# Optimization experiments

Measured on AMD Instinct MI355X. Metric: run time of the kernel, lower is better.

Reference implementation:

```python
import jax, jax.numpy as jnp
import numpy as np

# mamba-130m backbone dims. NOTE: the original torch code wires Conv1d(1,8,...) into a
# 768-d Mamba (a latent bug); we resolve it by making the downsample conv emit d_model.
B, L_IN = 2, 135000
D_MODEL, N_LAYERS = 768, 24
D_INNER, D_STATE, D_CONV, DT_RANK = 1536, 16, 4, 48
K_DS, S_DS = 32, 32
LATENT = 64


def setup_inputs() -> dict:
    key = jax.random.key(0)
    ks = jax.random.split(key, 16)
    s = 0.02
    dt = jax.random.uniform(ks[12], (N_LAYERS, D_INNER), minval=1e-3, maxval=1e-1)
    return {
        "x": jax.random.normal(ks[0], (B, 1, L_IN), dtype=jnp.float32),
        "conv_w": jax.random.normal(ks[1], (D_MODEL, 1, K_DS)) * s,
        "conv_b": jnp.zeros((D_MODEL,)),
        "norm_w": jnp.ones((N_LAYERS, D_MODEL)),
        "in_proj_w": jax.random.normal(ks[2], (N_LAYERS, 2 * D_INNER, D_MODEL)) * s,
        "conv1d_w": jax.random.normal(ks[3], (N_LAYERS, D_INNER, D_CONV)) * s,
        "conv1d_b": jnp.zeros((N_LAYERS, D_INNER)),
        "x_proj_w": jax.random.normal(ks[4], (N_LAYERS, DT_RANK + 2 * D_STATE, D_INNER)) * s,
        "dt_proj_w": jax.random.normal(ks[5], (N_LAYERS, D_INNER, DT_RANK)) * s,
        "dt_proj_b": dt + jnp.log(-jnp.expm1(-dt)),  # inverse-softplus init
        "A_log": jnp.log(jnp.broadcast_to(jnp.arange(1, D_STATE + 1, dtype=jnp.float32), (N_LAYERS, D_INNER, D_STATE)) + 0.0),
        "D_skip": jnp.ones((N_LAYERS, D_INNER)),
        "out_proj_w": jax.random.normal(ks[6], (N_LAYERS, D_MODEL, D_INNER)) * s,
        "norm_f_w": jnp.ones((D_MODEL,)),
        "proj_w": jax.random.normal(ks[7], (LATENT, D_MODEL)) * s,
        "proj_b": jnp.zeros((LATENT,)),
        "ln_w": jnp.ones((LATENT,)),
        "ln_b": jnp.zeros((LATENT,)),
    }


def _rmsnorm(x, w):
    return x * jax.lax.rsqrt(jnp.mean(x * x, axis=-1, keepdims=True) + 1e-5) * w


def _mamba_layer(h, p):
    norm_w, in_w, cw, cb, xp_w, dt_w, dt_b, A_log, Dp, out_w = p
    xz = jnp.einsum('btd,ed->bte', _rmsnorm(h, norm_w), in_w)  # e = 2*d_inner
    u, z = jnp.split(xz, 2, axis=-1)
    # causal depthwise conv over time
    uc = jax.lax.conv_general_dilated(jnp.transpose(u, (0, 2, 1)), cw[:, None, :], (1,),
                                      [(D_CONV - 1, 0)], dimension_numbers=('NCH', 'OIH', 'NCH'),
                                      feature_group_count=D_INNER)
    u = jax.nn.silu(jnp.transpose(uc + cb[None, :, None], (0, 2, 1)))  # (B,T,d_inner)
    proj = jnp.einsum('btd,ed->bte', u, xp_w)
    dt, Bm, Cm = jnp.split(proj, [DT_RANK, DT_RANK + D_STATE], axis=-1)
    delta = jax.nn.softplus(jnp.einsum('btr,dr->btd', dt, dt_w) + dt_b)
    A = -jnp.exp(A_log)  # (d_inner, d_state)

    def step(hc, inp):
        u_t, d_t, b_t, c_t = inp  # (B,d_inner),(B,d_inner),(B,d_state),(B,d_state)
        hc = jnp.exp(d_t[..., None] * A) * hc + (d_t * u_t)[..., None] * b_t[:, None, :]
        return hc, jnp.einsum('bds,bs->bd', hc, c_t)

    h0 = jnp.zeros((u.shape[0], D_INNER, D_STATE), dtype=u.dtype)
    tfirst = lambda a: jnp.transpose(a, (1, 0, 2))
    _, ys = jax.lax.scan(step, h0, (tfirst(u), tfirst(delta), tfirst(Bm), tfirst(Cm)))
    y = (jnp.transpose(ys, (1, 0, 2)) + u * Dp) * jax.nn.silu(z)
    return h + jnp.einsum('bte,de->btd', y, out_w), None


def _forward(x, conv_w, conv_b, norm_w, in_proj_w, conv1d_w, conv1d_b, x_proj_w, dt_proj_w,
             dt_proj_b, A_log, D_skip, out_proj_w, norm_f_w, proj_w, proj_b, ln_w, ln_b):
    # downsample: (B,1,135000) -> (B,768,4218) -> (B,4218,768)
    xds = jax.lax.conv_general_dilated(x, conv_w, (S_DS,), 'VALID',
                                       dimension_numbers=('NCH', 'OIH', 'NCH')) + conv_b[None, :, None]
    h = jnp.transpose(xds, (0, 2, 1))
    params = (norm_w, in_proj_w, conv1d_w, conv1d_b, x_proj_w, dt_proj_w, dt_proj_b, A_log, D_skip, out_proj_w)
    h, _ = jax.lax.scan(_mamba_layer, h, params)
    h = _rmsnorm(h, norm_f_w)  # last_hidden_state
    pooled = h.mean(axis=1)  # mean pooling
    zed = pooled @ proj_w.T + proj_b
    mu = zed.mean(-1, keepdims=True)
    var = ((zed - mu) ** 2).mean(-1, keepdims=True)
    return (zed - mu) * jax.lax.rsqrt(var + 1e-5) * ln_w + ln_b  # dropout is identity in eval


def reference(x, conv_w, conv_b, norm_w, in_proj_w, conv1d_w, conv1d_b, x_proj_w, dt_proj_w,
              dt_proj_b, A_log, D_skip, out_proj_w, norm_f_w, proj_w, proj_b, ln_w, ln_b):
    return _forward(x, conv_w, conv_b, norm_w, in_proj_w, conv1d_w, conv1d_b, x_proj_w,
                    dt_proj_w, dt_proj_b, A_log, D_skip, out_proj_w, norm_f_w, proj_w,
                    proj_b, ln_w, ln_b)
```

## Files before the change

### kernel.cpp

```cpp
#include <hip/hip_runtime.h>
#include <hip/hip_bf16.h>
#include <math.h>

#define TT 4218
#define BB 2
#define DM 768
#define DI 1536
#define DS 16
#define DTR 48
#define LC 64
#define NCHUNK 66
#define ROWS (BB*TT)
#define NLAYER 24

typedef short short8 __attribute__((ext_vector_type(8)));
typedef float f32x4 __attribute__((ext_vector_type(4)));

__device__ __forceinline__ float silu_f(float x) { return x / (1.0f + __expf(-x)); }
__device__ __forceinline__ float softplus_f(float x) {
  return (x > 15.0f) ? x : log1pf(__expf(x));
}
__device__ __forceinline__ unsigned short f2bf(float x) {
  unsigned int u = __float_as_uint(x);
  u = (u + 0x7fffu + ((u >> 16) & 1u)) >> 16;
  return (unsigned short)u;
}
__device__ __forceinline__ float bf2f(unsigned short s) {
  return __uint_as_float(((unsigned int)s) << 16);
}

__global__ __launch_bounds__(256)
void k_f2bf(const float4* __restrict__ in, ushort4* __restrict__ out, int n4) {
  int i = blockIdx.x*256 + threadIdx.x;
  if (i >= n4) return;
  float4 v = in[i];
  ushort4 o;
  o.x = f2bf(v.x); o.y = f2bf(v.y); o.z = f2bf(v.z); o.w = f2bf(v.w);
  out[i] = o;
}

__global__ __launch_bounds__(256)
void k_cvt_dtw(const float* __restrict__ in, unsigned short* __restrict__ out, int n) {
  int i = blockIdx.x*256 + threadIdx.x;
  if (i >= n) return;
  int col = i & 63, row = i >> 6;
  out[i] = (col < DTR) ? f2bf(in[row*DTR + col]) : (unsigned short)0;
}

__global__ __launch_bounds__(256)
void k_zero_dtpad(unsigned short* __restrict__ fdt) {
  int i = blockIdx.x*256 + threadIdx.x;
  if (i >= ROWS*16) return;
  int r = i >> 4, c = i & 15;
  fdt[(size_t)r*64 + DTR + c] = 0;
}

__global__ __launch_bounds__(256)
void k_conv_ds(const float* __restrict__ x, const float* __restrict__ cw,
               const float* __restrict__ cb, float* __restrict__ h) {
  int bt = blockIdx.x;
  int b = bt / TT, t = bt % TT;
  __shared__ float xs[32];
  int tid = threadIdx.x;
  if (tid < 32) xs[tid] = x[(size_t)b*135000 + (size_t)t*32 + tid];
  __syncthreads();
  for (int d = tid; d < DM; d += 256) {
    float s = cb[d];
    const float* w = cw + d*32;
    #pragma unroll
    for (int k = 0; k < 32; ++k) s = fmaf(xs[k], w[k], s);
    h[(size_t)bt*DM + d] = s;
  }
}

__global__ __launch_bounds__(256)
void k_rmsnorm(const float* __restrict__ in, const float* __restrict__ w,
               unsigned short* __restrict__ out) {
  int row = blockIdx.x, tid = threadIdx.x;
  const float* xp = in + (size_t)row*DM;
  float v0 = xp[tid], v1 = xp[tid+256], v2 = xp[tid+512];
  float ss = v0*v0 + v1*v1 + v2*v2;
  #pragma unroll
  for (int off = 32; off > 0; off >>= 1) ss += __shfl_down(ss, off, 64);
  __shared__ float sred[4];
  if ((tid & 63) == 0) sred[tid >> 6] = ss;
  __syncthreads();
  float tot = sred[0] + sred[1] + sred[2] + sred[3];
  float sc = rsqrtf(tot * (1.0f/DM) + 1e-5f);
  unsigned short* op = out + (size_t)row*DM;
  op[tid]     = f2bf(v0*sc*w[tid]);
  op[tid+256] = f2bf(v1*sc*w[tid+256]);
  op[tid+512] = f2bf(v2*sc*w[tid+512]);
}

#define GLL(g, l) __builtin_amdgcn_global_load_lds( \
    (const __attribute__((address_space(1))) void*)(g), \
    (__attribute__((address_space(3))) void*)(l), 16, 0, 0)

template<int MODE>
__global__ __launch_bounds__(256)
void k_gemm_bf(const unsigned short* __restrict__ A,
               const unsigned short* __restrict__ W,
               const float* __restrict__ bias,
               float* __restrict__ Cf,
               unsigned short* __restrict__ Cb0, unsigned short* __restrict__ Cb1,
               int ldc, int M, int N, int K) {
  const int m0 = blockIdx.x*128, n0 = blockIdx.y*128;
  if (m0 >= M) return;
  __shared__ unsigned short As[128*32];
  __shared__ unsigned short Ws[128*32];
  const int tid = threadIdx.x;
  const int lane = tid & 63;
  const int wave = tid >> 6;
  const int wm = (wave >> 1)*64, wn = (wave & 1)*64;

  const int sA = tid & 3;
  const int r0 = tid >> 2;
  const int r1 = r0 + 64;
  const int seg0 = sA ^ ((r0 >> 1) & 3);
  const int seg1 = sA ^ ((r1 >> 1) & 3);
  const unsigned short* gA0 = A + (size_t)min(m0+r0, M-1)*K + seg0*8;
  const unsigned short* gA1 = A + (size_t)min(m0+r1, M-1)*K + seg1*8;
  const unsigned short* gW0 = W + (size_t)min(n0+r0, N-1)*K + seg0*8;
  const unsigned short* gW1 = W + (size_t)min(n0+r1, N-1)*K + seg1*8;
  unsigned short* lA0 = As + tid*8;
  unsigned short* lA1 = As + (tid+256)*8;
  unsigned short* lW0 = Ws + tid*8;
  unsigned short* lW1 = Ws + (tid+256)*8;

  f32x4 acc[4][4];
  #pragma unroll
  for (int i = 0; i < 4; ++i)
    #pragma unroll
    for (int j = 0; j < 4; ++j) acc[i][j] = (f32x4){0.f,0.f,0.f,0.f};

  const int lr = lane & 15, kg = lane >> 4;
  const int sw = (kg ^ ((lr >> 1) & 3)) * 8;
  const int aoff = (wm + lr)*32 + sw;
  const int boff = (wn + lr)*32 + sw;

  for (int k0 = 0; k0 < K; k0 += 32) {
    GLL(gA0, lA0); GLL(gA1, lA1);
    GLL(gW0, lW0); GLL(gW1, lW1);
    gA0 += 32; gA1 += 32; gW0 += 32; gW1 += 32;
    __syncthreads();
    short8 af[4], bfr[4];
    #pragma unroll
    for (int i = 0; i < 4; ++i) {
      af[i]  = *(const short8*)(As + aoff + i*512);
      bfr[i] = *(const short8*)(Ws + boff + i*512);
    }
    #pragma unroll
    for (int i = 0; i < 4; ++i)
      #pragma unroll
      for (int j = 0; j < 4; ++j)
        acc[i][j] = __builtin_amdgcn_mfma_f32_16x16x32_bf16(af[i], bfr[j], acc[i][j], 0, 0, 0);
    __syncthreads();
  }

  #pragma unroll
  for (int i = 0; i < 4; ++i) {
    int gr0 = m0 + wm + i*16 + kg*4;
    #pragma unroll
    for (int j = 0; j < 4; ++j) {
      int gc = n0 + wn + j*16 + lr;
      if (gc >= N) continue;
      #pragma unroll
      for (int r = 0; r < 4; ++r) {
        int gr = gr0 + r;
        if (gr >= M) continue;
        float v = acc[i][j][r];
        if (MODE == 0) {
          if (gc < DI) Cb0[(size_t)gr*ldc + gc] = f2bf(v);
          else         Cb1[(size_t)gr*ldc + gc - DI] = f2bf(v);
        } else if (MODE == 1) {
          Cf[(size_t)gr*ldc + gc] += v;
        } else {
          Cf[(size_t)gr*ldc + gc] = softplus_f(v + bias[gc]);
        }
      }
    }
  }
}

__global__ __launch_bounds__(256)
void k_gemm_xp(const unsigned short* __restrict__ A,
               const unsigned short* __restrict__ W,
               float* __restrict__ Cpr, unsigned short* __restrict__ Cdt,
               int M) {
  __shared__ unsigned short As[64*64];
  __shared__ unsigned short Ws[80*64];
  const int tid = threadIdx.x;
  const int m0 = blockIdx.x*64;
  const int lane = tid & 63;
  const int wave = tid >> 6;
  const int K = DI;

  const int rA0 = tid >> 3,        gA0s = (tid & 7) ^ (rA0 & 7);
  const int rA1 = (tid+256) >> 3,  gA1s = ((tid+256) & 7) ^ (rA1 & 7);
  const unsigned short* gA0 = A + (size_t)min(m0+rA0, M-1)*K + gA0s*8;
  const unsigned short* gA1 = A + (size_t)min(m0+rA1, M-1)*K + gA1s*8;
  unsigned short* lA0 = As + tid*8;
  unsigned short* lA1 = As + (size_t)(tid+256)*8;
  const int rW0 = tid >> 3,        gW0s = (tid & 7) ^ (rW0 & 7);
  const int rW1 = (tid+256) >> 3,  gW1s = ((tid+256) & 7) ^ (rW1 & 7);
  const int rW2 = (tid+512) >> 3,  gW2s = ((tid+512) & 7) ^ (rW2 & 7);
  const unsigned short* gW0 = W + (size_t)rW0*K + gW0s*8;
  const unsigned short* gW1 = W + (size_t)rW1*K + gW1s*8;
  const unsigned short* gW2 = W + (size_t)min(rW2,79)*K + gW2s*8;
  unsigned short* lW0 = Ws + tid*8;
  unsigned short* lW1 = Ws + (size_t)(tid+256)*8;
  unsigned short* lW2 = Ws + (size_t)(tid+512)*8;
  const bool doW2 = (tid < 128);

  f32x4 acc[5];
  #pragma unroll
  for (int j = 0; j < 5; ++j) acc[j] = (f32x4){0.f,0.f,0.f,0.f};

  const int lr = lane & 15, kg = lane >> 4;
  const int rowA = wave*16 + lr;

  for (int k0 = 0; k0 < K; k0 += 64) {
    GLL(gA0, lA0); GLL(gA1, lA1);
    GLL(gW0, lW0); GLL(gW1, lW1);
    if (doW2) GLL(gW2, lW2);
    gA0 += 64; gA1 += 64; gW0 += 64; gW1 += 64; gW2 += 64;
    __syncthreads();
    #pragma unroll
    for (int ks = 0; ks < 2; ++ks) {
      const int G = ks*4 + kg;
      short8 af = *(const short8*)(As + ((size_t)rowA*8 + (G ^ (rowA & 7)))*8);
      #pragma unroll
      for (int j = 0; j < 5; ++j) {
        const int rw = j*16 + lr;
        short8 bf = *(const short8*)(Ws + ((size_t)rw*8 + (G ^ (rw & 7)))*8);
        acc[j] = __builtin_amdgcn_mfma_f32_16x16x32_bf16(af, bf, acc[j], 0, 0, 0);
      }
    }
    __syncthreads();
  }

  #pragma unroll
  for (int j = 0; j < 5; ++j) {
    int gc = j*16 + lr;
    #pragma unroll
    for (int r = 0; r < 4; ++r) {
      int gr = m0 + wave*16 + kg*4 + r;
      if (gr >= M) continue;
      float v = acc[j][r];
      Cpr[(size_t)gr*80 + gc] = v;
      if (gc < DTR) Cdt[(size_t)gr*64 + gc] = f2bf(v);
    }
  }
}

__global__ __launch_bounds__(256)
void k_dwconv(const unsigned short* __restrict__ U0, const float* __restrict__ cw,
              const float* __restrict__ cb, unsigned short* __restrict__ ubf) {
  size_t i4 = (size_t)blockIdx.x*256 + threadIdx.x;
  if (i4 >= (size_t)ROWS*DI/4) return;
  size_t base = i4*4;
  int d = (int)(base % DI);
  size_t bt = base / DI;
  int t = (int)(bt % TT);
  float4 cbv = *(const float4*)(cb + d);
  float s0 = cbv.x, s1 = cbv.y, s2 = cbv.z, s3 = cbv.w;
  float4 w0v = *(const float4*)(cw + (size_t)(d+0)*4);
  float4 w1v = *(const float4*)(cw + (size_t)(d+1)*4);
  float4 w2v = *(const float4*)(cw + (size_t)(d+2)*4);
  float4 w3v = *(const float4*)(cw + (size_t)(d+3)*4);
  const float* w0 = (const float*)&w0v;
  const float* w1 = (const float*)&w1v;
  const float* w2 = (const float*)&w2v;
  const float* w3 = (const float*)&w3v;
  #pragma unroll
  for (int k = 0; k < 4; ++k) {
    int tt = t - 3 + k;
    if (tt < 0) continue;
    ushort4 uu = *(const ushort4*)(U0 + (bt - 3 + k)*DI + d);
    s0 = fmaf(bf2f(uu.x), w0[k], s0);
    s1 = fmaf(bf2f(uu.y), w1[k], s1);
    s2 = fmaf(bf2f(uu.z), w2[k], s2);
    s3 = fmaf(bf2f(uu.w), w3[k], s3);
  }
  ushort4 o4;
  o4.x = f2bf(silu_f(s0)); o4.y = f2bf(silu_f(s1));
  o4.z = f2bf(silu_f(s2)); o4.w = f2bf(silu_f(s3));
  *(ushort4*)(ubf + base) = o4;
}

__global__ __launch_bounds__(256)
void k_scan1(const float* __restrict__ delta, const unsigned short* __restrict__ u,
             const float* __restrict__ proj, const float* __restrict__ A_log,
             float* __restrict__ P, float* __restrict__ H) {
  int c = blockIdx.x, b = blockIdx.z;
  int d = blockIdx.y * 256 + threadIdx.x;
  float A[DS];
  {
    const float4* a4 = (const float4*)(A_log + (size_t)d*DS);
    #pragma unroll
    for (int q = 0; q < 4; ++q) {
      float4 v = a4[q];
      A[q*4+0] = -__expf(v.x); A[q*4+1] = -__expf(v.y);
      A[q*4+2] = -__expf(v.z); A[q*4+3] = -__expf(v.w);
    }
  }
  float h[DS] = {};
  float sdl = 0.0f;
  int t0 = c * LC, t1 = min(t0 + LC, TT);
  for (int t = t0; t < t1; ++t) {
    size_t bt = (size_t)b*TT + t;
    float dl = delta[bt*DI + d];
    float du = dl * bf2f(u[bt*DI + d]);
    const float4* pb4 = (const float4*)(proj + bt*80 + DTR);
    float4 B0 = pb4[0], B1 = pb4[1], B2 = pb4[2], B3 = pb4[3];
    float Bv[DS] = {B0.x,B0.y,B0.z,B0.w, B1.x,B1.y,B1.z,B1.w,
                    B2.x,B2.y,B2.z,B2.w, B3.x,B3.y,B3.z,B3.w};
    sdl += dl;
    #pragma unroll
    for (int s = 0; s < DS; ++s) {
      float e = __expf(dl * A[s]);
      h[s] = fmaf(e, h[s], du * Bv[s]);
    }
  }
  size_t o = (((size_t)c*BB + b)*DI + d)*DS;
  #pragma unroll
  for (int q = 0; q < 4; ++q) {
    float4 pv, hv;
    pv.x = __expf(sdl*A[q*4+0]); pv.y = __expf(sdl*A[q*4+1]);
    pv.z = __expf(sdl*A[q*4+2]); pv.w = __expf(sdl*A[q*4+3]);
    hv.x = h[q*4+0]; hv.y = h[q*4+1]; hv.z = h[q*4+2]; hv.w = h[q*4+3];
    *(float4*)(P + o + q*4) = pv;
    *(float4*)(H + o + q*4) = hv;
  }
}

__global__ __launch_bounds__(256)
void k_scan2(float* __restrict__ P, float* __restrict__ H) {
  int i = blockIdx.x*256 + threadIdx.x;
  const size_t CH = (size_t)BB*DI*DS;
  size_t o = (size_t)i;
  float carry = 0.0f;
  float p0 = P[o],      h0 = H[o];
  float p1 = P[o + CH], h1 = H[o + CH];
  for (int c = 0; c < NCHUNK; ++c) {
    float p2 = 0.0f, h2 = 0.0f;
    if (c + 2 < NCHUNK) { size_t o2 = o + 2*CH; p2 = P[o2]; h2 = H[o2]; }
    H[o] = carry;
    carry = fmaf(p0, carry, h0);
    p0 = p1; h0 = h1; p1 = p2; h1 = h2;
    o += CH;
  }
}

__global__ __launch_bounds__(256)
void k_scan3(const float* __restrict__ delta, const unsigned short* __restrict__ u,
             const unsigned short* __restrict__ z, const float* __restrict__ proj,
             const float* __restrict__ A_log, const float* __restrict__ Dskip,
             const float* __restrict__ H, unsigned short* __restrict__ y) {
  int c = blockIdx.x, b = blockIdx.z;
  int d = blockIdx.y * 256 + threadIdx.x;
  float A[DS];
  {
    const float4* a4 = (const float4*)(A_log + (size_t)d*DS);
    #pragma unroll
    for (int q = 0; q < 4; ++q) {
      float4 v = a4[q];
      A[q*4+0] = -__expf(v.x); A[q*4+1] = -__expf(v.y);
      A[q*4+2] = -__expf(v.z); A[q*4+3] = -__expf(v.w);
    }
  }
  float h[DS];
  size_t o = (((size_t)c*BB + b)*DI + d)*DS;
  #pragma unroll
  for (int q = 0; q < 4; ++q) {
    float4 hv = *(const float4*)(H + o + q*4);
    h[q*4+0] = hv.x; h[q*4+1] = hv.y; h[q*4+2] = hv.z; h[q*4+3] = hv.w;
  }
  float Dd = Dskip[d];
  int t0 = c * LC, t1 = min(t0 + LC, TT);
  for (int t = t0; t < t1; ++t) {
    size_t bt = (size_t)b*TT + t;
    float dl = delta[bt*DI + d];
    float uu = bf2f(u[bt*DI + d]);
    float du = dl * uu;
    const float4* pb4 = (const float4*)(proj + bt*80 + DTR);
    float4 B0 = pb4[0], B1 = pb4[1], B2 = pb4[2], B3 = pb4[3];
    float4 C0 = pb4[4], C1 = pb4[5], C2 = pb4[6], C3 = pb4[7];
    float Bv[DS] = {B0.x,B0.y,B0.z,B0.w, B1.x,B1.y,B1.z,B1.w,
                    B2.x,B2.y,B2.z,B2.w, B3.x,B3.y,B3.z,B3.w};
    float Cv[DS] = {C0.x,C0.y,C0.z,C0.w, C1.x,C1.y,C1.z,C1.w,
                    C2.x,C2.y,C2.z,C2.w, C3.x,C3.y,C3.z,C3.w};
    float yt = 0.0f;
    #pragma unroll
    for (int s = 0; s < DS; ++s) {
      float e = __expf(dl * A[s]);
      h[s] = fmaf(e, h[s], du * Bv[s]);
      yt = fmaf(h[s], Cv[s], yt);
    }
    float zz = bf2f(z[bt*DI + d]);
    y[bt*DI + d] = f2bf((yt + uu*Dd) * silu_f(zz));
  }
}

__global__ __launch_bounds__(256)
void k_poolpart(const unsigned short* __restrict__ hn, float* __restrict__ pp) {
  int seg = blockIdx.x, b = blockIdx.z;
  int d = blockIdx.y*256 + threadIdx.x;
  int t0 = seg*132, t1 = min(t0 + 132, TT);
  float s = 0.0f;
  for (int t = t0; t < t1; ++t) s += bf2f(hn[((size_t)b*TT + t)*DM + d]);
  pp[((size_t)b*32 + seg)*DM + d] = s;
}

__global__ __launch_bounds__(256)
void k_head(const float* __restrict__ pp, const float* __restrict__ pw,
            const float* __restrict__ pb, const float* __restrict__ lnw,
            const float* __restrict__ lnb, float* __restrict__ out) {
  int b = blockIdx.x, tid = threadIdx.x;
  __shared__ float pooled[DM];
  for (int d = tid; d < DM; d += 256) {
    float s = 0.0f;
    for (int seg = 0; seg < 32; ++seg) s += pp[((size_t)b*32 + seg)*DM + d];
    pooled[d] = s * (1.0f/(float)TT);
  }
  __syncthreads();
  __shared__ float zed[64];
  if (tid < 64) {
    float s = pb[tid];
    const float* w = pw + (size_t)tid*DM;
    for (int d = 0; d < DM; ++d) s = fmaf(pooled[d], w[d], s);
    zed[tid] = s;
  }
  __syncthreads();
  __shared__ float mv[2];
  if (tid == 0) {
    float mu = 0.0f;
    for (int l = 0; l < 64; ++l) mu += zed[l];
    mu *= (1.0f/64.0f);
    float var = 0.0f;
    for (int l = 0; l < 64; ++l) { float dd = zed[l]-mu; var += dd*dd; }
    var *= (1.0f/64.0f);
    mv[0] = mu; mv[1] = rsqrtf(var + 1e-5f);
  }
  __syncthreads();
  if (tid < 64) out[b*64 + tid] = (zed[tid]-mv[0])*mv[1]*lnw[tid] + lnb[tid];
}

extern "C" void kernel_launch(void* const* d_in, const int* in_sizes, int n_in,
                              void* d_out, int out_size, void* d_ws, size_t ws_size,
                              hipStream_t stream) {
  (void)in_sizes; (void)n_in; (void)out_size; (void)ws_size;
  const float* x    = (const float*)d_in[0];
  const float* cw   = (const float*)d_in[1];
  const float* cb   = (const float*)d_in[2];
  const float* nw   = (const float*)d_in[3];
  const float* inw  = (const float*)d_in[4];
  const float* c1w  = (const float*)d_in[5];
  const float* c1b  = (const float*)d_in[6];
  const float* xpw  = (const float*)d_in[7];
  const float* dtw  = (const float*)d_in[8];
  const float* dtb  = (const float*)d_in[9];
  const float* alog = (const float*)d_in[10];
  const float* dsk  = (const float*)d_in[11];
  const float* outw = (const float*)d_in[12];
  const float* nfw  = (const float*)d_in[13];
  const float* pw   = (const float*)d_in[14];
  const float* pb   = (const float*)d_in[15];
  const float* lnw  = (const float*)d_in[16];
  const float* lnb  = (const float*)d_in[17];

  char* wsb = (char*)d_ws;
  size_t o = 0;
  float* f_h  = (float*)(wsb + o); o += (size_t)ROWS*DM*4;
  float* f_pr = (float*)(wsb + o); o += (size_t)ROWS*80*4;
  float* f_dl = (float*)(wsb + o); o += (size_t)ROWS*DI*4;
  float* f_P  = (float*)(wsb + o); o += (size_t)NCHUNK*BB*DI*DS*4;
  float* f_H  = (float*)(wsb + o); o += (size_t)NCHUNK*BB*DI*DS*4;
  float* f_pp = (float*)(wsb + o); o += (size_t)BB*32*DM*4;
  unsigned short* hn_bf = (unsigned short*)(wsb + o); o += (size_t)ROWS*DM*2;
  unsigned short* u0_bf = (unsigned short*)(wsb + o); o += (size_t)ROWS*DI*2;
  unsigned short* z_bf  = (unsigned short*)(wsb + o); o += (size_t)ROWS*DI*2;
  unsigned short* u_bf  = (unsigned short*)(wsb + o); o += (size_t)ROWS*DI*2;
  unsigned short* y_bf  = (unsigned short*)(wsb + o); o += (size_t)ROWS*DI*2;
  unsigned short* f_dt  = (unsigned short*)(wsb + o); o += (size_t)ROWS*64*2;
  unsigned short* w_in  = (unsigned short*)(wsb + o); o += (size_t)2*DI*DM*2;
  unsigned short* w_xp  = (unsigned short*)(wsb + o); o += (size_t)NLAYER*80*DI*2;
  unsigned short* w_out = (unsigned short*)(wsb + o); o += (size_t)NLAYER*DM*DI*2;
  unsigned short* w_dt  = (unsigned short*)(wsb + o); o += (size_t)NLAYER*DI*64*2;

  k_conv_ds<<<ROWS, 256, 0, stream>>>(x, cw, cb, f_h);
  k_f2bf<<<(NLAYER*80*DI/4+255)/256, 256, 0, stream>>>(
      (const float4*)xpw, (ushort4*)w_xp, NLAYER*80*DI/4);
  k_f2bf<<<(NLAYER*DM*DI/4+255)/256, 256, 0, stream>>>(
      (const float4*)outw, (ushort4*)w_out, NLAYER*DM*DI/4);
  k_cvt_dtw<<<(NLAYER*DI*64+255)/256, 256, 0, stream>>>(dtw, w_dt, NLAYER*DI*64);
  k_zero_dtpad<<<(ROWS*16+255)/256, 256, 0, stream>>>(f_dt);

  for (int lay = 0; lay < NLAYER; ++lay) {
    k_f2bf<<<(2*DI*DM/4+255)/256, 256, 0, stream>>>(
        (const float4*)(inw + (size_t)lay*2*DI*DM), (ushort4*)w_in, 2*DI*DM/4);
    k_rmsnorm<<<ROWS, 256, 0, stream>>>(f_h, nw + (size_t)lay*DM, hn_bf);
    k_gemm_bf<0><<<dim3(72,24), 256, 0, stream>>>(
        hn_bf, w_in, nullptr, nullptr, u0_bf, z_bf, DI, ROWS, 2*DI, DM);
    k_dwconv<<<(int)(((size_t)ROWS*DI/4+255)/256), 256, 0, stream>>>(
        u0_bf, c1w + (size_t)lay*DI*4, c1b + (size_t)lay*DI, u_bf);
    k_gemm_xp<<<132, 256, 0, stream>>>(
        u_bf, w_xp + (size_t)lay*80*DI, f_pr, f_dt, ROWS);
    k_gemm_bf<2><<<dim3(72,12), 256, 0, stream>>>(
        f_dt, w_dt + (size_t)lay*DI*64, dtb + (size_t)lay*DI,
        f_dl, nullptr, nullptr, DI, ROWS, DI, 64);
    k_scan1<<<dim3(NCHUNK,6,BB), 256, 0, stream>>>(
        f_dl, u_bf, f_pr, alog + (size_t)lay*DI*DS, f_P, f_H);
    k_scan2<<<dim3((BB*DI*DS)/256), 256, 0, stream>>>(f_P, f_H);
    k_scan3<<<dim3(NCHUNK,6,BB), 256, 0, stream>>>(
        f_dl, u_bf, z_bf, f_pr, alog + (size_t)lay*DI*DS,
        dsk + (size_t)lay*DI, f_H, y_bf);
    k_gemm_bf<1><<<dim3(72,6), 256, 0, stream>>>(
        y_bf, w_out + (size_t)lay*DM*DI, nullptr,
        f_h, nullptr, nullptr, DM, ROWS, DM, DI);
  }

  k_rmsnorm<<<ROWS, 256, 0, stream>>>(f_h, nfw, hn_bf);
  k_poolpart<<<dim3(32,3,BB), 256, 0, stream>>>(hn_bf, f_pp);
  k_head<<<BB, 256, 0, stream>>>(f_pp, pw, pb, lnw, lnb, (float*)d_out);
}
```

Before: 11.64 ms.

## Deepen GEMM K-tile, store chunk delta sums instead of decay, preconvert in_proj weights

The bf16 GEMM now stages a 64-wide K slice per iteration with an 8-segment XOR swizzle, which halves the number of barrier pairs per tile at the cost of twice the LDS. The chunked scan no longer writes a per-state decay tensor P. It writes only the per-channel delta sum and recomputes exp(sdl*A) inside scan2, which now uses 64-thread blocks. All 24 layers of in_proj weights are converted to bf16 once up front when the workspace is large enough, replacing a per-layer conversion launch.

Measured after the change: 10.11 ms. 13.2% less time.

```diff
diff --git a/kernel.cpp b/kernel.cpp
--- a/kernel.cpp
+++ b/kernel.cpp
@@ -107,26 +107,27 @@
                int ldc, int M, int N, int K) {
   const int m0 = blockIdx.x*128, n0 = blockIdx.y*128;
   if (m0 >= M) return;
-  __shared__ unsigned short As[128*32];
-  __shared__ unsigned short Ws[128*32];
+  __shared__ unsigned short As[128*64];
+  __shared__ unsigned short Ws[128*64];
   const int tid = threadIdx.x;
   const int lane = tid & 63;
   const int wave = tid >> 6;
   const int wm = (wave >> 1)*64, wn = (wave & 1)*64;
 
-  const int sA = tid & 3;
-  const int r0 = tid >> 2;
-  const int r1 = r0 + 64;
-  const int seg0 = sA ^ ((r0 >> 1) & 3);
-  const int seg1 = sA ^ ((r1 >> 1) & 3);
-  const unsigned short* gA0 = A + (size_t)min(m0+r0, M-1)*K + seg0*8;
-  const unsigned short* gA1 = A + (size_t)min(m0+r1, M-1)*K + seg1*8;
-  const unsigned short* gW0 = W + (size_t)min(n0+r0, N-1)*K + seg0*8;
-  const unsigned short* gW1 = W + (size_t)min(n0+r1, N-1)*K + seg1*8;
-  unsigned short* lA0 = As + tid*8;
-  unsigned short* lA1 = As + (tid+256)*8;
-  unsigned short* lW0 = Ws + tid*8;
-  unsigned short* lW1 = Ws + (tid+256)*8;
+  const unsigned short* gA[4];
+  const unsigned short* gW[4];
+  unsigned short* lA[4];
+  unsigned short* lW[4];
+  #pragma unroll
+  for (int i = 0; i < 4; ++i) {
+    int c = i*256 + tid;
+    int row = c >> 3;
+    int gs = (c & 7) ^ (row & 7);
+    gA[i] = A + (size_t)min(m0+row, M-1)*K + gs*8;
+    gW[i] = W + (size_t)min(n0+row, N-1)*K + gs*8;
+    lA[i] = As + (size_t)c*8;
+    lW[i] = Ws + (size_t)c*8;
+  }
 
   f32x4 acc[4][4];
   #pragma unroll
@@ -135,26 +136,32 @@
     for (int j = 0; j < 4; ++j) acc[i][j] = (f32x4){0.f,0.f,0.f,0.f};
 
   const int lr = lane & 15, kg = lane >> 4;
-  const int sw = (kg ^ ((lr >> 1) & 3)) * 8;
-  const int aoff = (wm + lr)*32 + sw;
-  const int boff = (wn + lr)*32 + sw;
-
-  for (int k0 = 0; k0 < K; k0 += 32) {
-    GLL(gA0, lA0); GLL(gA1, lA1);
-    GLL(gW0, lW0); GLL(gW1, lW1);
-    gA0 += 32; gA1 += 32; gW0 += 32; gW1 += 32;
+
+  for (int k0 = 0; k0 < K; k0 += 64) {
+    #pragma unroll
+    for (int i = 0; i < 4; ++i) GLL(gA[i], lA[i]);
+    #pragma unroll
+    for (int i = 0; i < 4; ++i) GLL(gW[i], lW[i]);
+    #pragma unroll
+    for (int i = 0; i < 4; ++i) { gA[i] += 64; gW[i] += 64; }
     __syncthreads();
-    short8 af[4], bfr[4];
-    #pragma unroll
-    for (int i = 0; i < 4; ++i) {
-      af[i]  = *(const short8*)(As + aoff + i*512);
-      bfr[i] = *(const short8*)(Ws + boff + i*512);
-    }
-    #pragma unroll
-    for (int i = 0; i < 4; ++i)
+    #pragma unroll
+    for (int kk = 0; kk < 2; ++kk) {
+      const int ks = kk*4 + kg;
+      short8 af[4], bfr[4];
       #pragma unroll
-      for (int j = 0; j < 4; ++j)
-        acc[i][j] = __builtin_amdgcn_mfma_f32_16x16x32_bf16(af[i], bfr[j], acc[i][j], 0, 0, 0);
+      for (int i = 0; i < 4; ++i) {
+        const int R  = wm + i*16 + lr;
+        const int Rw = wn + i*16 + lr;
+        af[i]  = *(const short8*)(As + ((size_t)R*8  + (ks ^ (R  & 7)))*8);
+        bfr[i] = *(const short8*)(Ws + ((size_t)Rw*8 + (ks ^ (Rw & 7)))*8);
+      }
+      #pragma unroll
+      for (int i = 0; i < 4; ++i)
+        #pragma unroll
+        for (int j = 0; j < 4; ++j)
+          acc[i][j] = __builtin_amdgcn_mfma_f32_16x16x32_bf16(af[i], bfr[j], acc[i][j], 0, 0, 0);
+    }
     __syncthreads();
   }
 
@@ -292,7 +299,7 @@
 __global__ __launch_bounds__(256)
 void k_scan1(const float* __restrict__ delta, const unsigned short* __restrict__ u,
              const float* __restrict__ proj, const float* __restrict__ A_log,
-             float* __restrict__ P, float* __restrict__ H) {
+             float* __restrict__ sdl_out, float* __restrict__ H) {
   int c = blockIdx.x, b = blockIdx.z;
   int d = blockIdx.y * 256 + threadIdx.x;
   float A[DS];
@@ -324,32 +331,37 @@
     }
   }
   size_t o = (((size_t)c*BB + b)*DI + d)*DS;
+  sdl_out[((size_t)c*BB + b)*DI + d] = sdl;
   #pragma unroll
   for (int q = 0; q < 4; ++q) {
-    float4 pv, hv;
-    pv.x = __expf(sdl*A[q*4+0]); pv.y = __expf(sdl*A[q*4+1]);
-    pv.z = __expf(sdl*A[q*4+2]); pv.w = __expf(sdl*A[q*4+3]);
+    float4 hv;
     hv.x = h[q*4+0]; hv.y = h[q*4+1]; hv.z = h[q*4+2]; hv.w = h[q*4+3];
-    *(float4*)(P + o + q*4) = pv;
     *(float4*)(H + o + q*4) = hv;
   }
 }
 
-__global__ __launch_bounds__(256)
-void k_scan2(float* __restrict__ P, float* __restrict__ H) {
-  int i = blockIdx.x*256 + threadIdx.x;
-  const size_t CH = (size_t)BB*DI*DS;
-  size_t o = (size_t)i;
+__global__ __launch_bounds__(64)
+void k_scan2(const float* __restrict__ sdl, const float* __restrict__ A_log,
+             float* __restrict__ H) {
+  int i = blockIdx.x*64 + threadIdx.x;
+  int s = i & 15;
+  int dd = (i >> 4) % DI;
+  int b = i / (DI*DS);
+  float As = -__expf(A_log[dd*DS + s]);
+  const size_t CH  = (size_t)BB*DI*DS;
+  const size_t CHD = (size_t)BB*DI;
+  size_t oh = (size_t)i;
+  size_t od = (size_t)b*DI + dd;
   float carry = 0.0f;
-  float p0 = P[o],      h0 = H[o];
-  float p1 = P[o + CH], h1 = H[o + CH];
+  float sd0 = sdl[od],       h0 = H[oh];
+  float sd1 = sdl[od + CHD], h1 = H[oh + CH];
   for (int c = 0; c < NCHUNK; ++c) {
-    float p2 = 0.0f, h2 = 0.0f;
-    if (c + 2 < NCHUNK) { size_t o2 = o + 2*CH; p2 = P[o2]; h2 = H[o2]; }
-    H[o] = carry;
-    carry = fmaf(p0, carry, h0);
-    p0 = p1; h0 = h1; p1 = p2; h1 = h2;
-    o += CH;
+    float sd2 = 0.0f, h2 = 0.0f;
+    if (c + 2 < NCHUNK) { sd2 = sdl[od + 2*CHD]; h2 = H[oh + 2*CH]; }
+    H[oh] = carry;
+    carry = fmaf(__expf(sd0*As), carry, h0);
+    sd0 = sd1; h0 = h1; sd1 = sd2; h1 = h2;
+    oh += CH; od += CHD;
   }
 }
 
@@ -450,7 +462,7 @@
 extern "C" void kernel_launch(void* const* d_in, const int* in_sizes, int n_in,
                               void* d_out, int out_size, void* d_ws, size_t ws_size,
                               hipStream_t stream) {
-  (void)in_sizes; (void)n_in; (void)out_size; (void)ws_size;
+  (void)in_sizes; (void)n_in; (void)out_size;
   const float* x    = (const float*)d_in[0];
   const float* cw   = (const float*)d_in[1];
   const float* cb   = (const float*)d_in[2];
@@ -472,12 +484,12 @@
 
   char* wsb = (char*)d_ws;
   size_t o = 0;
-  float* f_h  = (float*)(wsb + o); o += (size_t)ROWS*DM*4;
-  float* f_pr = (float*)(wsb + o); o += (size_t)ROWS*80*4;
-  float* f_dl = (float*)(wsb + o); o += (size_t)ROWS*DI*4;
-  float* f_P  = (float*)(wsb + o); o += (size_t)NCHUNK*BB*DI*DS*4;
-  float* f_H  = (float*)(wsb + o); o += (size_t)NCHUNK*BB*DI*DS*4;
-  float* f_pp = (float*)(wsb + o); o += (size_t)BB*32*DM*4;
+  float* f_h   = (float*)(wsb + o); o += (size_t)ROWS*DM*4;
+  float* f_pr  = (float*)(wsb + o); o += (size_t)ROWS*80*4;
+  float* f_dl  = (float*)(wsb + o); o += (size_t)ROWS*DI*4;
+  float* f_sdl = (float*)(wsb + o); o += (size_t)NCHUNK*BB*DI*4;
+  float* f_H   = (float*)(wsb + o); o += (size_t)NCHUNK*BB*DI*DS*4;
+  float* f_pp  = (float*)(wsb + o); o += (size_t)BB*32*DM*4;
   unsigned short* hn_bf = (unsigned short*)(wsb + o); o += (size_t)ROWS*DM*2;
   unsigned short* u0_bf = (unsigned short*)(wsb + o); o += (size_t)ROWS*DI*2;
   unsigned short* z_bf  = (unsigned short*)(wsb + o); o += (size_t)ROWS*DI*2;
@@ -488,6 +500,9 @@
   unsigned short* w_xp  = (unsigned short*)(wsb + o); o += (size_t)NLAYER*80*DI*2;
   unsigned short* w_out = (unsigned short*)(wsb + o); o += (size_t)NLAYER*DM*DI*2;
   unsigned short* w_dt  = (unsigned short*)(wsb + o); o += (size_t)NLAYER*DI*64*2;
+  size_t w_in_all_sz = (size_t)NLAYER*2*DI*DM*2;
+  unsigned short* w_in_all =
+      (ws_size >= o + w_in_all_sz) ? (unsigned short*)(wsb + o) : nullptr;
 
   k_conv_ds<<<ROWS, 256, 0, stream>>>(x, cw, cb, f_h);
   k_f2bf<<<(NLAYER*80*DI/4+255)/256, 256, 0, stream>>>(
@@ -496,13 +511,24 @@
       (const float4*)outw, (ushort4*)w_out, NLAYER*DM*DI/4);
   k_cvt_dtw<<<(NLAYER*DI*64+255)/256, 256, 0, stream>>>(dtw, w_dt, NLAYER*DI*64);
   k_zero_dtpad<<<(ROWS*16+255)/256, 256, 0, stream>>>(f_dt);
+  if (w_in_all) {
+    int n4 = NLAYER*2*DI*DM/4;
+    k_f2bf<<<(n4+255)/256, 256, 0, stream>>>(
+        (const float4*)inw, (ushort4*)w_in_all, n4);
+  }
 
   for (int lay = 0; lay < NLAYER; ++lay) {
-    k_f2bf<<<(2*DI*DM/4+255)/256, 256, 0, stream>>>(
-        (const float4*)(inw + (size_t)lay*2*DI*DM), (ushort4*)w_in, 2*DI*DM/4);
+    const unsigned short* w_in_l;
+    if (w_in_all) {
+      w_in_l = w_in_all + (size_t)lay*2*DI*DM;
+    } else {
+      k_f2bf<<<(2*DI*DM/4+255)/256, 256, 0, stream>>>(
+          (const float4*)(inw + (size_t)lay*2*DI*DM), (ushort4*)w_in, 2*DI*DM/4);
+      w_in_l = w_in;
+    }
     k_rmsnorm<<<ROWS, 256, 0, stream>>>(f_h, nw + (size_t)lay*DM, hn_bf);
     k_gemm_bf<0><<<dim3(72,24), 256, 0, stream>>>(
-        hn_bf, w_in, nullptr, nullptr, u0_bf, z_bf, DI, ROWS, 2*DI, DM);
+        hn_bf, w_in_l, nullptr, nullptr, u0_bf, z_bf, DI, ROWS, 2*DI, DM);
     k_dwconv<<<(int)(((size_t)ROWS*DI/4+255)/256), 256, 0, stream>>>(
         u0_bf, c1w + (size_t)lay*DI*4, c1b + (size_t)lay*DI, u_bf);
     k_gemm_xp<<<132, 256, 0, stream>>>(
@@ -511,8 +537,9 @@
         f_dt, w_dt + (size_t)lay*DI*64, dtb + (size_t)lay*DI,
         f_dl, nullptr, nullptr, DI, ROWS, DI, 64);
     k_scan1<<<dim3(NCHUNK,6,BB), 256, 0, stream>>>(
-        f_dl, u_bf, f_pr, alog + (size_t)lay*DI*DS, f_P, f_H);
-    k_scan2<<<dim3((BB*DI*DS)/256), 256, 0, stream>>>(f_P, f_H);
+        f_dl, u_bf, f_pr, alog + (size_t)lay*DI*DS, f_sdl, f_H);
+    k_scan2<<<dim3((BB*DI*DS)/64), 64, 0, stream>>>(
+        f_sdl, alog + (size_t)lay*DI*DS, f_H);
     k_scan3<<<dim3(NCHUNK,6,BB), 256, 0, stream>>>(
         f_dl, u_bf, z_bf, f_pr, alog + (size_t)lay*DI*DS,
         dsk + (size_t)lay*DI, f_H, y_bf);
```
